# Kernel tuning notes

Measured on AMD Instinct MI355X. Metric: run time of the kernel, lower is better.

Reference implementation:

```python
import jax, jax.numpy as jnp
import numpy as np

VOCAB, HID, EMB = 32000, 512, 100
DROPOUT = 0.3
BN_EPS = 1e-5


def setup_inputs() -> dict:
    key = jax.random.key(0)
    ks = jax.random.split(key, 12)
    B, T = 64, 512
    s = 1.0 / np.sqrt(HID)
    inp = {
        "x": jax.random.randint(ks[0], (B, T), 0, VOCAB),
        "emb_table": jax.random.normal(ks[1], (VOCAB, HID), jnp.float32) * 0.1,
        # PyTorch LSTMCell layout: weight_ih [4H, H], weight_hh [4H, H], gate order i,f,g,o
        "w_ih": jax.random.uniform(ks[2], (4 * HID, HID), jnp.float32, -s, s),
        "w_hh": jax.random.uniform(ks[3], (4 * HID, HID), jnp.float32, -s, s),
        "b_ih": jax.random.uniform(ks[4], (4 * HID,), jnp.float32, -s, s),
        "b_hh": jax.random.uniform(ks[5], (4 * HID,), jnp.float32, -s, s),
        "gamma": jnp.ones((HID,), jnp.float32),
        "beta": jnp.zeros((HID,), jnp.float32),
        "dec_w": jax.random.uniform(ks[6], (EMB, HID), jnp.float32, -s, s),
        "dec_b": jax.random.uniform(ks[7], (EMB,), jnp.float32, -s, s),
        # LockedDropout: one bernoulli(keep) mask shared across all timesteps
        "mask": jax.random.bernoulli(ks[8], 1.0 - DROPOUT, (B, HID)).astype(jnp.float32),
    }
    return inp


def reference(x, emb_table, w_ih, w_hh, b_ih, b_hh, gamma, beta, dec_w, dec_b, mask):
    embed = emb_table[x]                    # [B, T, H]
    xs = jnp.swapaxes(embed, 0, 1)          # [T, B, H]
    B = x.shape[0]
    keep = 1.0 - DROPOUT

    def step(carry, x_t):
        h, c = carry
        gates = x_t @ w_ih.T + b_ih + h @ w_hh.T + b_hh     # [B, 4H]
        i, f, g, o = jnp.split(gates, 4, axis=-1)
        i = jax.nn.sigmoid(i)
        f = jax.nn.sigmoid(f)
        g = jnp.tanh(g)
        o = jax.nn.sigmoid(o)
        c = f * c + i * g
        h = o * jnp.tanh(c)
        # BatchNorm1d in training mode: per-step batch stats (biased variance)
        mu = jnp.mean(h, axis=0)
        var = jnp.mean((h - mu) ** 2, axis=0)
        hn = (h - mu) * jax.lax.rsqrt(var + BN_EPS) * gamma + beta
        hd = hn * mask / keep                # LockedDropout, fixed mask
        out = hd @ dec_w.T + dec_b           # [B, EMB]
        return (h, c), out

    h0 = jnp.zeros((B, HID), embed.dtype)
    c0 = jnp.zeros((B, HID), embed.dtype)
    _, outs = jax.lax.scan(step, (h0, c0), xs)   # [T, B, EMB]
    # MaxPool1d with kernel == T over time axis -> max over T
    return jnp.max(outs, axis=0)                  # [B, EMB]
```

## Files before the change

### kernel.cpp

```cpp
#include <hip/hip_runtime.h>
#include <hip/hip_bf16.h>

#define TSEQ  512
#define BATCH 64
#define HIDN  512
#define EMBD  100
#define NWG   64

typedef __attribute__((ext_vector_type(8))) short short8;
typedef __attribute__((ext_vector_type(4))) float f32x4;
typedef unsigned int u32;

#define A_OFF   0ull
#define HD_OFF  33554432ull
#define HB_OFF  67108864ull
#define FLG_OFF 67239936ull
#define KEY_OFF 67244032ull
#define DW_OFF  67269632ull
#define ZERO_SPAN 160768ull

static __device__ __forceinline__ unsigned short f2bfbits(float f) {
    u32 u = __float_as_uint(f);
    u32 r = (u + 0x7fffu + ((u >> 16) & 1u)) >> 16;
    return (unsigned short)r;
}
static __device__ __forceinline__ float bf2f(unsigned short b) {
    return __uint_as_float(((u32)b) << 16);
}
static __device__ __forceinline__ float sigf(float x) {
    return __builtin_amdgcn_rcpf(1.0f + __expf(-x));
}
static __device__ __forceinline__ float tanhfast(float x) {
    float t = __expf(-2.0f * fabsf(x));
    float r = (1.0f - t) * __builtin_amdgcn_rcpf(1.0f + t);
    return copysignf(r, x);
}

__global__ void k_dw(const float* __restrict__ dw, unsigned short* __restrict__ dwb) {
    int i = blockIdx.x * 256 + threadIdx.x;
    float v = (i < EMBD * HIDN) ? dw[i] : 0.0f;
    dwb[i] = f2bfbits(v);
}

__global__ void k_embed(const int* __restrict__ x, const float* __restrict__ emb,
                        unsigned short* __restrict__ A) {
    int g = blockIdx.x * 256 + threadIdx.x;
    int k8 = g & 63;
    int bt = g >> 6;
    int b  = bt & 63;
    int t  = bt >> 6;
    int row = x[b * TSEQ + t];
    const float4* src = reinterpret_cast<const float4*>(emb + (size_t)row * HIDN + k8 * 8);
    float4 v0 = src[0], v1 = src[1];
    short8 s;
    s[0] = (short)f2bfbits(v0.x); s[1] = (short)f2bfbits(v0.y);
    s[2] = (short)f2bfbits(v0.z); s[3] = (short)f2bfbits(v0.w);
    s[4] = (short)f2bfbits(v1.x); s[5] = (short)f2bfbits(v1.y);
    s[6] = (short)f2bfbits(v1.z); s[7] = (short)f2bfbits(v1.w);
    *reinterpret_cast<short8*>(A + (size_t)g * 8) = s;
}

__launch_bounds__(512)
__global__ void k_lstm(const float* __restrict__ wih, const float* __restrict__ whh,
                       const float* __restrict__ bih, const float* __restrict__ bhh,
                       const unsigned short* __restrict__ A,
                       unsigned short* __restrict__ hbuf,
                       unsigned short* __restrict__ hd,
                       u32* __restrict__ flg) {
    const int tid  = threadIdx.x;
    const int wg   = blockIdx.x;
    const int g    = wg & 3;
    const int m    = wg >> 2;
    const int lane = tid & 63;
    const int w    = tid >> 6;
    const int nbw  = w & 3;
    const int kh   = w >> 2;

    __shared__ float gbuf[2][16][132];
    __shared__ __align__(16) unsigned short hstage[2][16][32];

    const int l15 = lane & 15;
    const int lk8 = (lane >> 4) * 8;

    const float* wsrc = kh ? whh : wih;
    short8 bfr[16][2];
    #pragma unroll
    for (int kk = 0; kk < 16; ++kk) {
        #pragma unroll
        for (int nb = 0; nb < 2; ++nb) {
            int jrow = nbw * HIDN + m * 32 + nb * 16 + l15;
            const float* p = wsrc + (size_t)jrow * HIDN + kk * 32 + lk8;
            short8 bb;
            #pragma unroll
            for (int e = 0; e < 8; ++e) bb[e] = (short)f2bfbits(p[e]);
            bfr[kk][nb] = bb;
        }
    }

    const int prow = tid >> 5;
    const int pcol = tid & 31;
    const int jj   = m * 32 + pcol;
    const float bias_i = bih[jj]           + bhh[jj];
    const float bias_f = bih[512 + jj]     + bhh[512 + jj];
    const float bias_g = bih[1024 + jj]    + bhh[1024 + jj];
    const float bias_o = bih[1536 + jj]    + bhh[1536 + jj];
    float c = 0.0f;

    const int arow = g * 16 + l15;
    const u32* fpoll = flg + ((size_t)g * 16 + (lane & 15)) * 16;

    {
        float* g1 = &gbuf[1][0][0];
        for (int i = tid; i < 16 * 132; i += 512) g1[i] = 0.0f;
    }
    __syncthreads();
    if (kh == 0) {
        const unsigned short* abase = A + (size_t)arow * HIDN;
        f32x4 a0 = {0.f,0.f,0.f,0.f}, a1 = {0.f,0.f,0.f,0.f};
        #pragma unroll
        for (int kk = 0; kk < 16; ++kk) {
            short8 a = *reinterpret_cast<const short8*>(abase + kk * 32 + lk8);
            a0 = __builtin_amdgcn_mfma_f32_16x16x32_bf16(a, bfr[kk][0], a0, 0, 0, 0);
            a1 = __builtin_amdgcn_mfma_f32_16x16x32_bf16(a, bfr[kk][1], a1, 0, 0, 0);
        }
        #pragma unroll
        for (int r = 0; r < 4; ++r) {
            int crow = (lane >> 4) * 4 + r;
            gbuf[0][crow][nbw * 32 + l15]      = a0[r];
            gbuf[0][crow][nbw * 32 + 16 + l15] = a1[r];
        }
    }
    __syncthreads();

    for (int s = 0; s < TSEQ; ++s) {
        float gi = gbuf[0][prow][pcol]      + gbuf[1][prow][pcol]      + bias_i;
        float gf = gbuf[0][prow][32 + pcol] + gbuf[1][prow][32 + pcol] + bias_f;
        float gg = gbuf[0][prow][64 + pcol] + gbuf[1][prow][64 + pcol] + bias_g;
        float go = gbuf[0][prow][96 + pcol] + gbuf[1][prow][96 + pcol] + bias_o;
        float iv = sigf(gi), fv = sigf(gf), gv = tanhfast(gg), ov = sigf(go);
        c = fv * c + iv * gv;
        float h = ov * tanhfast(c);
        hstage[s & 1][prow][pcol] = f2bfbits(h);
        __syncthreads();

        const int last = (s == TSEQ - 1);
        const int sb   = (s + 1) & 1;
        const u32 tgt  = (u32)(s + 1);

        if (!last && w == 0) {
            int r0 = lane >> 2, pc = (lane & 3) * 8;
            short8 hv = *reinterpret_cast<const short8*>(&hstage[s & 1][r0][pc]);
            unsigned short* dst = hbuf + ((size_t)(sb * 4 + g) * 16 + r0) * HIDN + m * 32 + pc;
            asm volatile("global_store_dwordx4 %0, %1, off sc1" :: "v"(dst), "v"(hv) : "memory");
            asm volatile("s_waitcnt vmcnt(0)" ::: "memory");
            if (lane == 0) {
                const u32* myf = flg + ((size_t)g * 16 + m) * 16;
                asm volatile("global_store_dword %0, %1, off sc1" :: "v"(myf), "v"(tgt) : "memory");
            }
        }

        if (w == 1) {
            int r0 = lane >> 2, pc = (lane & 3) * 8;
            short8 dv = *reinterpret_cast<const short8*>(&hstage[s & 1][r0][pc]);
            *reinterpret_cast<short8*>(
                hd + ((size_t)s * 64 + g * 16 + r0) * HIDN + m * 32 + pc) = dv;
        }

        if (!last) {
            if (kh == 0) {
                const unsigned short* abase = A + ((size_t)(s + 1) * 64 + arow) * HIDN;
                f32x4 a0 = {0.f,0.f,0.f,0.f}, a1 = {0.f,0.f,0.f,0.f};
                #pragma unroll
                for (int kk = 0; kk < 16; ++kk) {
                    short8 a = *reinterpret_cast<const short8*>(abase + kk * 32 + lk8);
                    a0 = __builtin_amdgcn_mfma_f32_16x16x32_bf16(a, bfr[kk][0], a0, 0, 0, 0);
                    a1 = __builtin_amdgcn_mfma_f32_16x16x32_bf16(a, bfr[kk][1], a1, 0, 0, 0);
                }
                #pragma unroll
                for (int r = 0; r < 4; ++r) {
                    int crow = (lane >> 4) * 4 + r;
                    gbuf[0][crow][nbw * 32 + l15]      = a0[r];
                    gbuf[0][crow][nbw * 32 + 16 + l15] = a1[r];
                }
            } else {
                u32 v;
                do {
                    asm volatile("global_load_dword %0, %1, off sc1"
                                 : "=v"(v) : "v"(fpoll) : "memory");
                    asm volatile("s_waitcnt vmcnt(0)" ::: "memory");
                } while (!__all((int)(v >= tgt)));
                __builtin_amdgcn_sched_barrier(0);
                const unsigned short* hbase = hbuf + ((size_t)(sb * 4 + g) * 16 + l15) * HIDN;
                short8 hf[16];
                #pragma unroll
                for (int kk = 0; kk < 16; ++kk) {
                    const unsigned short* p = hbase + kk * 32 + lk8;
                    asm volatile("global_load_dwordx4 %0, %1, off sc1"
                                 : "=v"(hf[kk]) : "v"(p) : "memory");
                }
                asm volatile("s_waitcnt vmcnt(0)" ::: "memory");
                __builtin_amdgcn_sched_barrier(0);
                f32x4 a0 = {0.f,0.f,0.f,0.f}, a1 = {0.f,0.f,0.f,0.f};
                #pragma unroll
                for (int kk = 0; kk < 16; ++kk) {
                    a0 = __builtin_amdgcn_mfma_f32_16x16x32_bf16(hf[kk], bfr[kk][0], a0, 0, 0, 0);
                    a1 = __builtin_amdgcn_mfma_f32_16x16x32_bf16(hf[kk], bfr[kk][1], a1, 0, 0, 0);
                }
                #pragma unroll
                for (int r = 0; r < 4; ++r) {
                    int crow = (lane >> 4) * 4 + r;
                    gbuf[1][crow][nbw * 32 + l15]      = a0[r];
                    gbuf[1][crow][nbw * 32 + 16 + l15] = a1[r];
                }
            }
        }
        __syncthreads();
    }
}

__launch_bounds__(256)
__global__ void k_bnd(const unsigned short* __restrict__ hd,
                      const unsigned short* __restrict__ dwb,
                      const float* __restrict__ gamma, const float* __restrict__ beta,
                      const float* __restrict__ mask,
                      u32* __restrict__ key) {
    const int t   = blockIdx.x;
    const int tid = threadIdx.x;
    __shared__ __align__(16) unsigned short hs[64][520];

    for (int ch = tid; ch < 4096; ch += 256) {
        int row = ch >> 6, c8 = (ch & 63) * 8;
        short8 v = *reinterpret_cast<const short8*>(hd + ((size_t)t * 64 + row) * HIDN + c8);
        *reinterpret_cast<short8*>(&hs[row][c8]) = v;
    }
    __syncthreads();

    {
        int c0 = tid * 2;
        float s10 = 0.f, s20 = 0.f, s11 = 0.f, s21 = 0.f;
        for (int r = 0; r < 64; ++r) {
            float x0 = bf2f(hs[r][c0]), x1 = bf2f(hs[r][c0 + 1]);
            s10 += x0; s20 += x0 * x0;
            s11 += x1; s21 += x1 * x1;
        }
        float mu0 = s10 * (1.0f / 64.0f), var0 = s20 * (1.0f / 64.0f) - mu0 * mu0;
        float mu1 = s11 * (1.0f / 64.0f), var1 = s21 * (1.0f / 64.0f) - mu1 * mu1;
        float sc0 = gamma[c0]     * rsqrtf(var0 + 1e-5f);
        float sc1 = gamma[c0 + 1] * rsqrtf(var1 + 1e-5f);
        float sh0 = beta[c0]     - mu0 * sc0;
        float sh1 = beta[c0 + 1] - mu1 * sc1;
        for (int r = 0; r < 64; ++r) {
            float2 mk = *reinterpret_cast<const float2*>(&mask[(size_t)r * HIDN + c0]);
            float y0 = (bf2f(hs[r][c0])     * sc0 + sh0) * mk.x * (1.0f / 0.7f);
            float y1 = (bf2f(hs[r][c0 + 1]) * sc1 + sh1) * mk.y * (1.0f / 0.7f);
            hs[r][c0]     = f2bfbits(y0);
            hs[r][c0 + 1] = f2bfbits(y1);
        }
    }
    __syncthreads();

    const int lane = tid & 63;
    const int w    = tid >> 6;
    const int l15  = lane & 15;
    const int lk8  = (lane >> 4) * 8;
    f32x4 acc[7];
    #pragma unroll
    for (int nb = 0; nb < 7; ++nb) acc[nb] = (f32x4){0.f, 0.f, 0.f, 0.f};
    #pragma unroll
    for (int kk = 0; kk < 16; ++kk) {
        short8 a = *reinterpret_cast<const short8*>(&hs[w * 16 + l15][kk * 32 + lk8]);
        #pragma unroll
        for (int nb = 0; nb < 7; ++nb) {
            short8 b = *reinterpret_cast<const short8*>(
                dwb + (size_t)(nb * 16 + l15) * HIDN + kk * 32 + lk8);
            acc[nb] = __builtin_amdgcn_mfma_f32_16x16x32_bf16(a, b, acc[nb], 0, 0, 0);
        }
    }
    #pragma unroll
    for (int nb = 0; nb < 7; ++nb) {
        int n = nb * 16 + l15;
        if (n < EMBD) {
            #pragma unroll
            for (int r = 0; r < 4; ++r) {
                int b = w * 16 + (lane >> 4) * 4 + r;
                u32 u  = __float_as_uint(acc[nb][r]);
                u32 kv = (u & 0x80000000u) ? ~u : (u | 0x80000000u);
                atomicMax(&key[b * EMBD + n], kv);
            }
        }
    }
}

__global__ void k_final(const u32* __restrict__ key, const float* __restrict__ db,
                        float* __restrict__ out) {
    int i = blockIdx.x * 256 + threadIdx.x;
    if (i < BATCH * EMBD) {
        u32 k = key[i];
        u32 u = (k & 0x80000000u) ? (k & 0x7fffffffu) : ~k;
        out[i] = __uint_as_float(u) + db[i % EMBD];
    }
}

extern "C" void kernel_launch(void* const* d_in, const int* in_sizes, int n_in,
                              void* d_out, int out_size, void* d_ws, size_t ws_size,
                              hipStream_t stream) {
    const int*   x   = (const int*)d_in[0];
    const float* emb = (const float*)d_in[1];
    const float* wih = (const float*)d_in[2];
    const float* whh = (const float*)d_in[3];
    const float* bih = (const float*)d_in[4];
    const float* bhh = (const float*)d_in[5];
    const float* gam = (const float*)d_in[6];
    const float* bet = (const float*)d_in[7];
    const float* dw  = (const float*)d_in[8];
    const float* db  = (const float*)d_in[9];
    const float* msk = (const float*)d_in[10];

    char* ws = (char*)d_ws;
    unsigned short* A   = (unsigned short*)(ws + A_OFF);
    unsigned short* hd  = (unsigned short*)(ws + HD_OFF);
    unsigned short* hb  = (unsigned short*)(ws + HB_OFF);
    u32*            flg = (u32*)(ws + FLG_OFF);
    u32*            key = (u32*)(ws + KEY_OFF);
    unsigned short* dwb = (unsigned short*)(ws + DW_OFF);

    hipMemsetAsync(ws + HB_OFF, 0, ZERO_SPAN, stream);
    k_dw    <<<224,  256, 0, stream>>>(dw, dwb);
    k_embed <<<8192, 256, 0, stream>>>(x, emb, A);
    k_lstm  <<<NWG,  512, 0, stream>>>(wih, whh, bih, bhh, A, hb, hd, flg);
    k_bnd   <<<TSEQ, 256, 0, stream>>>(hd, dwb, gam, bet, msk, key);
    k_final <<<25,   256, 0, stream>>>(key, db, (float*)d_out);
}
```

Measured before the change: 2.588 ms.

## Embed step tags alongside h values to replace flag polling with speculative loads

```diff
diff --git a/kernel.cpp b/kernel.cpp
--- a/kernel.cpp
+++ b/kernel.cpp
@@ -10,14 +10,16 @@
 typedef __attribute__((ext_vector_type(8))) short short8;
 typedef __attribute__((ext_vector_type(4))) float f32x4;
 typedef unsigned int u32;
+typedef __attribute__((ext_vector_type(4))) u32 u32x4;
+typedef __attribute__((ext_vector_type(2))) u32 u32x2;
 
 #define A_OFF   0ull
 #define HD_OFF  33554432ull
 #define HB_OFF  67108864ull
-#define FLG_OFF 67239936ull
-#define KEY_OFF 67244032ull
-#define DW_OFF  67269632ull
-#define ZERO_SPAN 160768ull
+#define FLG_OFF 67371008ull
+#define KEY_OFF 67375104ull
+#define DW_OFF  67400704ull
+#define ZERO_SPAN 291840ull
 
 static __device__ __forceinline__ unsigned short f2bfbits(float f) {
     u32 u = __float_as_uint(f);
@@ -64,7 +66,7 @@
 __global__ void k_lstm(const float* __restrict__ wih, const float* __restrict__ whh,
                        const float* __restrict__ bih, const float* __restrict__ bhh,
                        const unsigned short* __restrict__ A,
-                       unsigned short* __restrict__ hbuf,
+                       u32* __restrict__ hx,
                        unsigned short* __restrict__ hd,
                        u32* __restrict__ flg) {
     const int tid  = threadIdx.x;
@@ -78,6 +80,7 @@
 
     __shared__ float gbuf[2][16][132];
     __shared__ __align__(16) unsigned short hstage[2][16][32];
+    __shared__ __align__(16) unsigned short h_lds[16][520];
 
     const int l15 = lane & 15;
     const int lk8 = (lane >> 4) * 8;
@@ -108,6 +111,8 @@
 
     const int arow = g * 16 + l15;
     const u32* fpoll = flg + ((size_t)g * 16 + (lane & 15)) * 16;
+    const int rr   = nbw * 4 + (lane >> 4);
+    const int lgrp = lane & 15;
 
     {
         float* g1 = &gbuf[1][0][0];
@@ -148,10 +153,14 @@
         const u32 tgt  = (u32)(s + 1);
 
         if (!last && w == 0) {
-            int r0 = lane >> 2, pc = (lane & 3) * 8;
-            short8 hv = *reinterpret_cast<const short8*>(&hstage[s & 1][r0][pc]);
-            unsigned short* dst = hbuf + ((size_t)(sb * 4 + g) * 16 + r0) * HIDN + m * 32 + pc;
-            asm volatile("global_store_dwordx4 %0, %1, off sc1" :: "v"(dst), "v"(hv) : "memory");
+            int row = lane >> 2, c0 = (lane & 3) * 8;
+            const u32* hrow = reinterpret_cast<const u32*>(&hstage[s & 1][row][c0]);
+            u32 d0 = hrow[0], d1 = hrow[1], d2 = hrow[2], d3 = hrow[3];
+            u32x4 q0 = {d0, tgt, d1, tgt};
+            u32x4 q1 = {d2, tgt, d3, tgt};
+            u32* dst = hx + (((size_t)sb * 4 + g) * 16 + row) * 512 + m * 32 + (lane & 3) * 8;
+            asm volatile("global_store_dwordx4 %0, %1, off sc1" :: "v"(dst), "v"(q0) : "memory");
+            asm volatile("global_store_dwordx4 %0, %1, off sc1" :: "v"(dst + 4), "v"(q1) : "memory");
             asm volatile("s_waitcnt vmcnt(0)" ::: "memory");
             if (lane == 0) {
                 const u32* myf = flg + ((size_t)g * 16 + m) * 16;
@@ -183,35 +192,77 @@
                     gbuf[0][crow][nbw * 32 + 16 + l15] = a1[r];
                 }
             } else {
-                u32 v;
-                do {
-                    asm volatile("global_load_dword %0, %1, off sc1"
-                                 : "=v"(v) : "v"(fpoll) : "memory");
-                    asm volatile("s_waitcnt vmcnt(0)" ::: "memory");
-                } while (!__all((int)(v >= tgt)));
-                __builtin_amdgcn_sched_barrier(0);
-                const unsigned short* hbase = hbuf + ((size_t)(sb * 4 + g) * 16 + l15) * HIDN;
-                short8 hf[16];
+                const size_t rowbase = (((size_t)sb * 4 + g) * 16 + rr) * 512;
+                u32x4 gq[8];
                 #pragma unroll
-                for (int kk = 0; kk < 16; ++kk) {
-                    const unsigned short* p = hbase + kk * 32 + lk8;
+                for (int q = 0; q < 8; ++q) {
+                    const u32* p = hx + rowbase + (q * 16 + lgrp) * 4;
                     asm volatile("global_load_dwordx4 %0, %1, off sc1"
-                                 : "=v"(hf[kk]) : "v"(p) : "memory");
+                                 : "=v"(gq[q]) : "v"(p) : "memory");
                 }
                 asm volatile("s_waitcnt vmcnt(0)" ::: "memory");
                 __builtin_amdgcn_sched_barrier(0);
-                f32x4 a0 = {0.f,0.f,0.f,0.f}, a1 = {0.f,0.f,0.f,0.f};
+                int ok;
+                {
+                    int o = 1;
+                    #pragma unroll
+                    for (int q = 0; q < 8; ++q) o &= (gq[q].y == tgt) & (gq[q].w == tgt);
+                    ok = __all(o);
+                }
+                #pragma unroll 1
+                for (int att = 0; att < 4 && !ok; ++att) {
+                    #pragma unroll
+                    for (int q = 0; q < 8; ++q) {
+                        const u32* p = hx + rowbase + (q * 16 + lgrp) * 4;
+                        asm volatile("global_load_dwordx4 %0, %1, off sc1"
+                                     : "=v"(gq[q]) : "v"(p) : "memory");
+                    }
+                    asm volatile("s_waitcnt vmcnt(0)" ::: "memory");
+                    __builtin_amdgcn_sched_barrier(0);
+                    int o = 1;
+                    #pragma unroll
+                    for (int q = 0; q < 8; ++q) o &= (gq[q].y == tgt) & (gq[q].w == tgt);
+                    ok = __all(o);
+                }
+                if (!ok) {
+                    u32 v;
+                    do {
+                        asm volatile("global_load_dword %0, %1, off sc1"
+                                     : "=v"(v) : "v"(fpoll) : "memory");
+                        asm volatile("s_waitcnt vmcnt(0)" ::: "memory");
+                    } while (!__all((int)(v >= tgt)));
+                    __builtin_amdgcn_sched_barrier(0);
+                    #pragma unroll
+                    for (int q = 0; q < 8; ++q) {
+                        const u32* p = hx + rowbase + (q * 16 + lgrp) * 4;
+                        asm volatile("global_load_dwordx4 %0, %1, off sc1"
+                                     : "=v"(gq[q]) : "v"(p) : "memory");
+                    }
+                    asm volatile("s_waitcnt vmcnt(0)" ::: "memory");
+                    __builtin_amdgcn_sched_barrier(0);
+                }
                 #pragma unroll
-                for (int kk = 0; kk < 16; ++kk) {
-                    a0 = __builtin_amdgcn_mfma_f32_16x16x32_bf16(hf[kk], bfr[kk][0], a0, 0, 0, 0);
-                    a1 = __builtin_amdgcn_mfma_f32_16x16x32_bf16(hf[kk], bfr[kk][1], a1, 0, 0, 0);
-                }
-                #pragma unroll
-                for (int r = 0; r < 4; ++r) {
-                    int crow = (lane >> 4) * 4 + r;
-                    gbuf[1][crow][nbw * 32 + l15]      = a0[r];
-                    gbuf[1][crow][nbw * 32 + 16 + l15] = a1[r];
-                }
+                for (int q = 0; q < 8; ++q) {
+                    u32x2 d = {gq[q].x, gq[q].z};
+                    *reinterpret_cast<u32x2*>(&h_lds[rr][(q * 16 + lgrp) * 4]) = d;
+                }
+            }
+        }
+        __syncthreads();
+
+        if (!last && kh == 1) {
+            f32x4 a0 = {0.f,0.f,0.f,0.f}, a1 = {0.f,0.f,0.f,0.f};
+            #pragma unroll
+            for (int kk = 0; kk < 16; ++kk) {
+                short8 a = *reinterpret_cast<const short8*>(&h_lds[l15][kk * 32 + lk8]);
+                a0 = __builtin_amdgcn_mfma_f32_16x16x32_bf16(a, bfr[kk][0], a0, 0, 0, 0);
+                a1 = __builtin_amdgcn_mfma_f32_16x16x32_bf16(a, bfr[kk][1], a1, 0, 0, 0);
+            }
+            #pragma unroll
+            for (int r = 0; r < 4; ++r) {
+                int crow = (lane >> 4) * 4 + r;
+                gbuf[1][crow][nbw * 32 + l15]      = a0[r];
+                gbuf[1][crow][nbw * 32 + 16 + l15] = a1[r];
             }
         }
         __syncthreads();
@@ -319,7 +370,7 @@
     char* ws = (char*)d_ws;
     unsigned short* A   = (unsigned short*)(ws + A_OFF);
     unsigned short* hd  = (unsigned short*)(ws + HD_OFF);
-    unsigned short* hb  = (unsigned short*)(ws + HB_OFF);
+    u32*            hx  = (u32*)(ws + HB_OFF);
     u32*            flg = (u32*)(ws + FLG_OFF);
     u32*            key = (u32*)(ws + KEY_OFF);
     unsigned short* dwb = (unsigned short*)(ws + DW_OFF);
@@ -327,7 +378,7 @@
     hipMemsetAsync(ws + HB_OFF, 0, ZERO_SPAN, stream);
     k_dw    <<<224,  256, 0, stream>>>(dw, dwb);
     k_embed <<<8192, 256, 0, stream>>>(x, emb, A);
-    k_lstm  <<<NWG,  512, 0, stream>>>(wih, whh, bih, bhh, A, hb, hd, flg);
+    k_lstm  <<<NWG,  512, 0, stream>>>(wih, whh, bih, bhh, A, hx, hd, flg);
     k_bnd   <<<TSEQ, 256, 0, stream>>>(hd, dwb, gam, bet, msk, key);
     k_final <<<25,   256, 0, stream>>>(key, db, (float*)d_out);
 }
```

After: 2.173 ms. 16.1% less time.
